# Performance work log

Measured on AMD Instinct MI355X. Metric: run time of the kernel, lower is better.

## Reference

```python
import jax, jax.numpy as jnp
import numpy as np

B, H_RES, W_RES, C, WS, SHIFT, NH = 32, 64, 64, 256, 8, 4, 8
N = WS * WS              # tokens per window
HD = C // NH             # head dim
HID = 4 * C              # mlp hidden
CPB_HID = 512            # relative-position MLP hidden


def _rel_index():
    coords = np.stack(np.meshgrid(np.arange(WS), np.arange(WS), indexing='ij'))  # [2,WS,WS]
    cf = coords.reshape(2, -1)
    rel = (cf[:, :, None] - cf[:, None, :]).transpose(1, 2, 0).astype(np.int64)  # [n,n,2]
    rel[..., 0] += WS - 1
    rel[..., 1] += WS - 1
    rel[..., 0] *= 2 * WS - 1
    return rel.sum(-1)  # [n,n] indices into (2WS-1)^2 table

REL_INDEX = _rel_index()


def _attn_mask():
    img = np.zeros((H_RES, W_RES))
    slices = (slice(0, -WS), slice(-WS, -SHIFT), slice(-SHIFT, None))
    cnt = 0
    for hs in slices:
        for ws_ in slices:
            img[hs, ws_] = cnt
            cnt += 1
    mw = img.reshape(H_RES // WS, WS, W_RES // WS, WS).transpose(0, 2, 1, 3).reshape(-1, N)
    am = mw[:, None, :] - mw[:, :, None]  # [nw,n,n]
    return np.where(am != 0, -100.0, 0.0).astype(np.float32)

ATTN_MASK = _attn_mask()


def _cpb_table():
    r = np.arange(-(WS - 1), WS, dtype=np.float32)
    t = np.stack(np.meshgrid(r, r, indexing='ij'), axis=-1)[None]  # [1,2WS-1,2WS-1,2]
    t = t / (WS - 1) * 8.0
    t = np.sign(t) * np.log2(np.abs(t) + 1.0) / np.log2(8.0)
    return t.astype(np.float32)

CPB_TABLE = _cpb_table()


def setup_inputs() -> dict:
    key = jax.random.key(0)
    ks = jax.random.split(key, 10)
    s = 0.02
    return {
        'x': jax.random.normal(ks[0], (B, H_RES * W_RES, C), jnp.float32),
        'qkv_w': jax.random.normal(ks[1], (3 * C, C), jnp.float32) * s,
        'q_bias': jnp.zeros((C,), jnp.float32),
        'v_bias': jnp.zeros((C,), jnp.float32),
        'logit_scale': jnp.full((NH, 1, 1), jnp.log(10.0), jnp.float32),
        'cpb_w1': jax.random.normal(ks[2], (CPB_HID, 2), jnp.float32) * s,
        'cpb_b1': jnp.zeros((CPB_HID,), jnp.float32),
        'cpb_w2': jax.random.normal(ks[3], (NH, CPB_HID), jnp.float32) * s,
        'proj_w': jax.random.normal(ks[4], (C, C), jnp.float32) * s,
        'proj_b': jnp.zeros((C,), jnp.float32),
        'norm1_g': jnp.ones((C,), jnp.float32),
        'norm1_b': jnp.zeros((C,), jnp.float32),
        'norm2_g': jnp.ones((C,), jnp.float32),
        'norm2_b': jnp.zeros((C,), jnp.float32),
        'fc1_w': jax.random.normal(ks[5], (HID, C), jnp.float32) * s,
        'fc1_b': jnp.zeros((HID,), jnp.float32),
        'fc2_w': jax.random.normal(ks[6], (C, HID), jnp.float32) * s,
        'fc2_b': jnp.zeros((C,), jnp.float32),
    }


def _layernorm(x, g, b, eps=1e-5):
    m = jnp.mean(x, axis=-1, keepdims=True)
    v = jnp.mean(jnp.square(x - m), axis=-1, keepdims=True)
    return (x - m) * jax.lax.rsqrt(v + eps) * g + b


def _l2norm(x, eps=1e-12):
    n = jnp.sqrt(jnp.sum(jnp.square(x), axis=-1, keepdims=True))
    return x / jnp.maximum(n, eps)


def reference(x, qkv_w, q_bias, v_bias, logit_scale, cpb_w1, cpb_b1, cpb_w2,
              proj_w, proj_b, norm1_g, norm1_b, norm2_g, norm2_b,
              fc1_w, fc1_b, fc2_w, fc2_b):
    shortcut = x
    xv = x.reshape(B, H_RES, W_RES, C)
    # cyclic shift
    sx = jnp.roll(xv, (-SHIFT, -SHIFT), axis=(1, 2))
    # window partition -> [B*nw, N, C]
    win = sx.reshape(B, H_RES // WS, WS, W_RES // WS, WS, C)
    win = win.transpose(0, 1, 3, 2, 4, 5).reshape(-1, N, C)

    # qkv with zero k-bias
    qkv_bias = jnp.concatenate([q_bias, jnp.zeros_like(v_bias), v_bias])
    qkv = win @ qkv_w.T + qkv_bias
    qkv = qkv.reshape(-1, N, 3, NH, HD).transpose(2, 0, 3, 1, 4)  # [3,Bw,NH,N,HD]
    q, k, v = qkv[0], qkv[1], qkv[2]

    # cosine attention with clamped learnable temperature
    attn = jnp.einsum('whnd,whmd->whnm', _l2norm(q), _l2norm(k))
    scale = jnp.exp(jnp.minimum(logit_scale, jnp.log(100.0)))  # [NH,1,1]
    attn = attn * scale

    # continuous relative position bias via MLP
    table = jnp.asarray(CPB_TABLE)  # [1,2WS-1,2WS-1,2]
    hmid = jax.nn.relu(table @ cpb_w1.T + cpb_b1)
    bias_table = (hmid @ cpb_w2.T).reshape(-1, NH)  # [(2WS-1)^2, NH]
    rpb = bias_table[jnp.asarray(REL_INDEX).reshape(-1)].reshape(N, N, NH)
    rpb = jax.nn.sigmoid(rpb.transpose(2, 0, 1)) * 16.0  # [NH,N,N]
    attn = attn + rpb[None]

    # shift mask
    mask = jnp.asarray(ATTN_MASK)  # [nw,N,N]
    nw = mask.shape[0]
    attn = attn.reshape(-1, nw, NH, N, N) + mask[None, :, None]
    attn = attn.reshape(-1, NH, N, N)
    attn = jax.nn.softmax(attn, axis=-1)

    out = jnp.einsum('whnm,whmd->whnd', attn, v).transpose(0, 2, 1, 3).reshape(-1, N, C)
    out = out @ proj_w.T + proj_b

    # window reverse + reverse shift
    out = out.reshape(B, H_RES // WS, W_RES // WS, WS, WS, C)
    out = out.transpose(0, 1, 3, 2, 4, 5).reshape(B, H_RES, W_RES, C)
    out = jnp.roll(out, (SHIFT, SHIFT), axis=(1, 2)).reshape(B, H_RES * W_RES, C)

    # post-norm residual (Swin v2 style)
    x1 = shortcut + _layernorm(out, norm1_g, norm1_b)
    mlp_out = jax.nn.gelu(x1 @ fc1_w.T + fc1_b, approximate=False) @ fc2_w.T + fc2_b
    x2 = x1 + _layernorm(mlp_out, norm2_g, norm2_b)
    return x2
```

## Files before the change

kernel.cpp:

```cpp
#include <hip/hip_runtime.h>

typedef unsigned short u16;
typedef unsigned int u32;
typedef __attribute__((ext_vector_type(8))) short bf16x8;
typedef __attribute__((ext_vector_type(4))) float f32x4;

#define CC_    256
#define NHD_   8
#define NT_    64
#define HD_    32
#define HID_   1024
#define CPBH_  512
#define BW_    2048
#define TOK_   131072
#define SHIFT_ 4

__device__ __forceinline__ int region9(int ph, int pw) {
  return (ph < 56 ? 0 : (ph < 60 ? 3 : 6)) + (pw < 56 ? 0 : (pw < 60 ? 1 : 2));
}
__device__ __forceinline__ float dot32(const float* qr, const float* krow) {
  float d0 = 0.f, d1 = 0.f, d2 = 0.f, d3 = 0.f;
#pragma unroll
  for (int d = 0; d < HD_; d += 4) {
    float4 kk = *reinterpret_cast<const float4*>(krow + d);
    d0 += qr[d] * kk.x; d1 += qr[d + 1] * kk.y;
    d2 += qr[d + 2] * kk.z; d3 += qr[d + 3] * kk.w;
  }
  return (d0 + d1) + (d2 + d3);
}

__device__ __forceinline__ u16 f2bf(float f) {
  u32 u = __builtin_bit_cast(u32, f);
  u = (u + 0x7FFFu + ((u >> 16) & 1u)) >> 16;
  return (u16)u;
}

__device__ __forceinline__ void split4(float4 f, uint2& hi, uint2& lo) {
  u16 h0 = f2bf(f.x), h1 = f2bf(f.y), h2 = f2bf(f.z), h3 = f2bf(f.w);
  float r0 = f.x - __builtin_bit_cast(float, (u32)h0 << 16);
  float r1 = f.y - __builtin_bit_cast(float, (u32)h1 << 16);
  float r2 = f.z - __builtin_bit_cast(float, (u32)h2 << 16);
  float r3 = f.w - __builtin_bit_cast(float, (u32)h3 << 16);
  hi = make_uint2((u32)h0 | ((u32)h1 << 16), (u32)h2 | ((u32)h3 << 16));
  lo = make_uint2((u32)f2bf(r0) | ((u32)f2bf(r1) << 16),
                  (u32)f2bf(r2) | ((u32)f2bf(r3) << 16));
}

__global__ void cpb_kernel(const float* __restrict__ w1, const float* __restrict__ b1,
                           const float* __restrict__ w2, float* __restrict__ bias_table) {
  __shared__ float hid[CPBH_];
  int p = blockIdx.x;
  int k = threadIdx.x;
  int hi = p / 15, wi = p % 15;
  float a0 = (float)(hi - 7) / 7.0f * 8.0f;
  float a1 = (float)(wi - 7) / 7.0f * 8.0f;
  float t0 = (a0 == 0.0f) ? 0.0f : copysignf(log2f(fabsf(a0) + 1.0f) / 3.0f, a0);
  float t1 = (a1 == 0.0f) ? 0.0f : copysignf(log2f(fabsf(a1) + 1.0f) / 3.0f, a1);
  float h = t0 * w1[2 * k] + t1 * w1[2 * k + 1] + b1[k];
  hid[k] = fmaxf(h, 0.0f);
  __syncthreads();
  if (k < NHD_) {
    float s = 0.0f;
    for (int j = 0; j < CPBH_; j++) s += hid[j] * w2[k * CPBH_ + j];
    bias_table[p * NHD_ + k] = s;
  }
}

__global__ void rpb_kernel(const float* __restrict__ bias_table, float* __restrict__ rpb) {
  int h = blockIdx.x >> 6;
  int i = blockIdx.x & 63;
  int j = threadIdx.x;
  int dih = (i >> 3) - (j >> 3) + 7;
  int diw = (i & 7) - (j & 7) + 7;
  float v = bias_table[(dih * 15 + diw) * NHD_ + h];
  rpb[(((h << 6) + i) << 6) + j] = 16.0f / (1.0f + expf(-v));
}

__global__ void convw_kernel(const float* __restrict__ w, u16* __restrict__ o, int n) {
  int i = blockIdx.x * 256 + threadIdx.x;
  if (i < n) o[i] = f2bf(w[i]);
}

__global__ void convsplit_kernel(const float* __restrict__ w, u16* __restrict__ hi,
                                 u16* __restrict__ lo, int n) {
  int i = blockIdx.x * 256 + threadIdx.x;
  if (i < n) {
    float v = w[i];
    u16 h = f2bf(v);
    hi[i] = h;
    lo[i] = f2bf(v - __builtin_bit_cast(float, (u32)h << 16));
  }
}

__global__ __launch_bounds__(512) void qkv_mfma_kernel(
    const float* __restrict__ x,
    const u16* __restrict__ wh_, const u16* __restrict__ wl_,
    const float* __restrict__ qb, const float* __restrict__ vb,
    float* __restrict__ qo, float* __restrict__ ko, float* __restrict__ vo, int w0) {
  __shared__ u16 xh[64 * 256];
  __shared__ u16 xl[64 * 256];
  int tid = threadIdx.x;
  int lane = tid & 63, wid = tid >> 6;
  int lr = lane & 15, lk = lane >> 4;
  int wl2 = blockIdx.x;
  int w = w0 + wl2;
  int b = w >> 6, win = w & 63, wwh = win >> 3, www = win & 7;

#pragma unroll
  for (int i = 0; i < 8; i++) {
    int idx = tid + i * 512;
    int n = idx >> 6, c4 = idx & 63;
    int sh = wwh * 8 + (n >> 3), sw = www * 8 + (n & 7);
    int hh = (sh + SHIFT_) & 63, wc = (sw + SHIFT_) & 63;
    float4 f = *reinterpret_cast<const float4*>(
        x + ((size_t)((b << 12) + (hh << 6) + wc)) * CC_ + c4 * 4);
    uint2 hi, lo; split4(f, hi, lo);
    int u = c4 >> 1;
    int off16 = n * 256 + ((u ^ (n & 7)) << 3) + ((c4 & 1) << 2);
    *reinterpret_cast<uint2*>(&xh[off16]) = hi;
    *reinterpret_cast<uint2*>(&xl[off16]) = lo;
  }
  __syncthreads();

  f32x4 acc[4][6];
#pragma unroll
  for (int m = 0; m < 4; m++)
#pragma unroll
    for (int nf = 0; nf < 6; nf++) acc[m][nf] = (f32x4){0.f, 0.f, 0.f, 0.f};

  for (int k0 = 0; k0 < CC_; k0 += 32) {
    int u0 = (k0 >> 3) + lk;
    bf16x8 ah[4], al[4];
#pragma unroll
    for (int m = 0; m < 4; m++) {
      int row = m * 16 + lr;
      int off16 = row * 256 + ((u0 ^ (row & 7)) << 3);
      ah[m] = *reinterpret_cast<const bf16x8*>(&xh[off16]);
      al[m] = *reinterpret_cast<const bf16x8*>(&xl[off16]);
    }
#pragma unroll
    for (int nf = 0; nf < 6; nf++) {
      int col = wid * 96 + nf * 16 + lr;
      size_t wo = (size_t)col * CC_ + k0 + lk * 8;
      bf16x8 bh = *reinterpret_cast<const bf16x8*>(wh_ + wo);
      bf16x8 bl = *reinterpret_cast<const bf16x8*>(wl_ + wo);
#pragma unroll
      for (int m = 0; m < 4; m++) {
        acc[m][nf] = __builtin_amdgcn_mfma_f32_16x16x32_bf16(ah[m], bh, acc[m][nf], 0, 0, 0);
        acc[m][nf] = __builtin_amdgcn_mfma_f32_16x16x32_bf16(al[m], bh, acc[m][nf], 0, 0, 0);
        acc[m][nf] = __builtin_amdgcn_mfma_f32_16x16x32_bf16(ah[m], bl, acc[m][nf], 0, 0, 0);
      }
    }
  }

#pragma unroll
  for (int nf = 0; nf < 6; nf++) {
    int col = wid * 96 + nf * 16 + lr;
    int mat = col >> 8, cc = col & 255;
    float bias = (mat == 0) ? qb[cc] : ((mat == 2) ? vb[cc] : 0.f);
    float* dst = (mat == 0) ? qo : ((mat == 1) ? ko : vo);
    int hd = cc >> 5, d = cc & 31;
    float* dp = dst + ((size_t)(wl2 * NHD_ + hd) * NT_) * HD_ + d;
#pragma unroll
    for (int m = 0; m < 4; m++)
#pragma unroll
      for (int r = 0; r < 4; r++) {
        int n = m * 16 + lk * 4 + r;
        dp[(size_t)n * HD_] = acc[m][nf][r] + bias;
      }
  }
}

__global__ __launch_bounds__(64) void attn_kernel(
    const float* __restrict__ qq, const float* __restrict__ kk_, const float* __restrict__ vv_,
    const float* __restrict__ ls, const float* __restrict__ rpb, float* __restrict__ attn_out, int w0) {
  __shared__ float ks[NT_][HD_];
  __shared__ float vs[NT_][HD_];
  int bid = blockIdx.x;
  int wl = bid >> 3, h = bid & 7;
  int w = w0 + wl;
  int i = threadIdx.x;
  size_t base = (size_t)bid * (NT_ * HD_) + (size_t)i * HD_;

  float qr[HD_];
  float ss = 0.f;
#pragma unroll
  for (int d = 0; d < HD_; d += 4) {
    float4 f = *reinterpret_cast<const float4*>(qq + base + d);
    qr[d] = f.x; qr[d + 1] = f.y; qr[d + 2] = f.z; qr[d + 3] = f.w;
    ss += f.x * f.x + f.y * f.y + f.z * f.z + f.w * f.w;
  }
  float inv = 1.0f / fmaxf(sqrtf(ss), 1e-12f);
#pragma unroll
  for (int d = 0; d < HD_; d++) qr[d] *= inv;

  float kr[HD_]; ss = 0.f;
#pragma unroll
  for (int d = 0; d < HD_; d += 4) {
    float4 f = *reinterpret_cast<const float4*>(kk_ + base + d);
    kr[d] = f.x; kr[d + 1] = f.y; kr[d + 2] = f.z; kr[d + 3] = f.w;
    ss += f.x * f.x + f.y * f.y + f.z * f.z + f.w * f.w;
  }
  inv = 1.0f / fmaxf(sqrtf(ss), 1e-12f);
#pragma unroll
  for (int d = 0; d < HD_; d += 4) {
    float4 t; t.x = kr[d] * inv; t.y = kr[d + 1] * inv; t.z = kr[d + 2] * inv; t.w = kr[d + 3] * inv;
    *reinterpret_cast<float4*>(&ks[i][d]) = t;
  }
#pragma unroll
  for (int d = 0; d < HD_; d += 4) {
    float4 f = *reinterpret_cast<const float4*>(vv_ + base + d);
    *reinterpret_cast<float4*>(&vs[i][d]) = f;
  }
  __syncthreads();

  float scale = expf(fminf(ls[h], 4.605170185988091f));
  const float* rp = rpb + (((h << 6) + i) << 6);
  int win = w & 63, wh = win >> 3, ww = win & 7;
  int regi = region9(wh * 8 + (i >> 3), ww * 8 + (i & 7));

  float m = -1e30f, l = 0.f;
  for (int j = 0; j < NT_; j++) {
    float dot = dot32(qr, &ks[j][0]);
    int regj = region9(wh * 8 + (j >> 3), ww * 8 + (j & 7));
    float val = dot * scale + rp[j] + (regj == regi ? 0.f : -100.f);
    float nm = fmaxf(m, val);
    l = l * expf(m - nm) + expf(val - nm);
    m = nm;
  }
  float rl = 1.0f / l;

  float acc[HD_];
#pragma unroll
  for (int d = 0; d < HD_; d++) acc[d] = 0.f;
  for (int j = 0; j < NT_; j++) {
    float dot = dot32(qr, &ks[j][0]);
    int regj = region9(wh * 8 + (j >> 3), ww * 8 + (j & 7));
    float val = dot * scale + rp[j] + (regj == regi ? 0.f : -100.f);
    float p = expf(val - m) * rl;
#pragma unroll
    for (int d = 0; d < HD_; d += 4) {
      float4 vvv = *reinterpret_cast<const float4*>(&vs[j][d]);
      acc[d] += p * vvv.x; acc[d + 1] += p * vvv.y; acc[d + 2] += p * vvv.z; acc[d + 3] += p * vvv.w;
    }
  }
  float* op = attn_out + ((size_t)(wl * NT_ + i)) * CC_ + h * HD_;
#pragma unroll
  for (int d = 0; d < HD_; d += 4) {
    float4 t; t.x = acc[d]; t.y = acc[d + 1]; t.z = acc[d + 2]; t.w = acc[d + 3];
    *reinterpret_cast<float4*>(op + d) = t;
  }
}

__global__ __launch_bounds__(512) void proj_mfma_kernel(
    const float* __restrict__ attn_out,
    const u16* __restrict__ pwh, const u16* __restrict__ pwl, const float* __restrict__ pb,
    const float* __restrict__ g, const float* __restrict__ bb,
    const float* __restrict__ x, float* __restrict__ x1, int w0) {
  __shared__ union {
    struct { u16 ah[64 * 256]; u16 al[64 * 256]; } s;
    float po[64][CC_];
  } sm;
  int tid = threadIdx.x;
  int lane = tid & 63, wid = tid >> 6;
  int lr = lane & 15, lk = lane >> 4;
  int wl2 = blockIdx.x;
  int w = w0 + wl2;

#pragma unroll
  for (int i = 0; i < 8; i++) {
    int idx = tid + i * 512;
    int n = idx >> 6, c4 = idx & 63;
    float4 f = *reinterpret_cast<const float4*>(
        attn_out + ((size_t)(wl2 * NT_ + n)) * CC_ + c4 * 4);
    uint2 hi, lo; split4(f, hi, lo);
    int u = c4 >> 1;
    int off16 = n * 256 + ((u ^ (n & 7)) << 3) + ((c4 & 1) << 2);
    *reinterpret_cast<uint2*>(&sm.s.ah[off16]) = hi;
    *reinterpret_cast<uint2*>(&sm.s.al[off16]) = lo;
  }
  __syncthreads();

  f32x4 acc[4][2];
#pragma unroll
  for (int m = 0; m < 4; m++)
#pragma unroll
    for (int nf = 0; nf < 2; nf++) acc[m][nf] = (f32x4){0.f, 0.f, 0.f, 0.f};

  for (int k0 = 0; k0 < CC_; k0 += 32) {
    int u0 = (k0 >> 3) + lk;
    bf16x8 ah[4], al[4];
#pragma unroll
    for (int m = 0; m < 4; m++) {
      int row = m * 16 + lr;
      int off16 = row * 256 + ((u0 ^ (row & 7)) << 3);
      ah[m] = *reinterpret_cast<const bf16x8*>(&sm.s.ah[off16]);
      al[m] = *reinterpret_cast<const bf16x8*>(&sm.s.al[off16]);
    }
#pragma unroll
    for (int nf = 0; nf < 2; nf++) {
      int col = wid * 32 + nf * 16 + lr;
      size_t wo = (size_t)col * CC_ + k0 + lk * 8;
      bf16x8 bh = *reinterpret_cast<const bf16x8*>(pwh + wo);
      bf16x8 bl = *reinterpret_cast<const bf16x8*>(pwl + wo);
#pragma unroll
      for (int m = 0; m < 4; m++) {
        acc[m][nf] = __builtin_amdgcn_mfma_f32_16x16x32_bf16(ah[m], bh, acc[m][nf], 0, 0, 0);
        acc[m][nf] = __builtin_amdgcn_mfma_f32_16x16x32_bf16(al[m], bh, acc[m][nf], 0, 0, 0);
        acc[m][nf] = __builtin_amdgcn_mfma_f32_16x16x32_bf16(ah[m], bl, acc[m][nf], 0, 0, 0);
      }
    }
  }
  __syncthreads();

#pragma unroll
  for (int nf = 0; nf < 2; nf++) {
    int col = wid * 32 + nf * 16 + lr;
    float bv = pb[col];
#pragma unroll
    for (int m = 0; m < 4; m++)
#pragma unroll
      for (int r = 0; r < 4; r++)
        sm.po[m * 16 + lk * 4 + r][col] = acc[m][nf][r] + bv;
  }
  __syncthreads();

  int t = wid * 8 + (lane >> 3);
  int j8 = ((lane & 7) + (lane >> 3)) & 7;
  float4 pv[8];
  float sum = 0.f, sq = 0.f;
#pragma unroll
  for (int i = 0; i < 8; i++) {
    float4 v = *reinterpret_cast<const float4*>(&sm.po[t][j8 * 4 + i * 32]);
    pv[i] = v;
    sum += v.x + v.y + v.z + v.w;
    sq += v.x * v.x + v.y * v.y + v.z * v.z + v.w * v.w;
  }
#pragma unroll
  for (int off = 1; off < 8; off <<= 1) {
    sum += __shfl_xor(sum, off, 8);
    sq  += __shfl_xor(sq, off, 8);
  }
  float mean = sum * (1.0f / CC_);
  float var = sq * (1.0f / CC_) - mean * mean;
  float rs = rsqrtf(fmaxf(var, 0.0f) + 1e-5f);
  int b = w >> 6, win = w & 63, wwh = win >> 3, www = win & 7;
  int sh = wwh * 8 + (t >> 3), sw = www * 8 + (t & 7);
  int hh = (sh + SHIFT_) & 63, wc = (sw + SHIFT_) & 63;
  size_t tok = ((size_t)(b << 12)) + (hh << 6) + wc;
  const float* xrow = x + tok * CC_;
  float* orow = x1 + tok * CC_;
#pragma unroll
  for (int i = 0; i < 8; i++) {
    int c = j8 * 4 + i * 32;
    float4 xg = *reinterpret_cast<const float4*>(xrow + c);
    float4 gg = *reinterpret_cast<const float4*>(g + c);
    float4 bv = *reinterpret_cast<const float4*>(bb + c);
    float4 r;
    r.x = xg.x + (pv[i].x - mean) * rs * gg.x + bv.x;
    r.y = xg.y + (pv[i].y - mean) * rs * gg.y + bv.y;
    r.z = xg.z + (pv[i].z - mean) * rs * gg.z + bv.z;
    r.w = xg.w + (pv[i].w - mean) * rs * gg.w + bv.w;
    *reinterpret_cast<float4*>(orow + c) = r;
  }
}

#define BM_   64

__global__ __launch_bounds__(512) void mlp_mfma_kernel(
    const float* __restrict__ x1,
    const u16* __restrict__ w1bf, const float* __restrict__ b1,
    const u16* __restrict__ w2bf, const float* __restrict__ b2,
    const float* __restrict__ g, const float* __restrict__ bb,
    float* __restrict__ out) {
  __shared__ union {
    struct { u16 xs[64 * 256]; u16 hid[2][64 * 128]; } s;
    float po[BM_][CC_];
  } sm;

  int tid = threadIdx.x;
  int lane = tid & 63;
  int wid = tid >> 6;
  int lr = lane & 15;
  int lk = lane >> 4;
  int whid = wid >> 1;
  int wtok = wid & 1;
  int wout = wid >> 1;
  int wtk2 = wid & 1;
  size_t t0 = (size_t)blockIdx.x * BM_;

#pragma unroll
  for (int i = 0; i < 8; i++) {
    int idx = tid + i * 512;
    int row = idx >> 6;
    int c4 = idx & 63;
    float4 f = *reinterpret_cast<const float4*>(x1 + (t0 + row) * CC_ + c4 * 4);
    u32 p0 = (u32)f2bf(f.x) | ((u32)f2bf(f.y) << 16);
    u32 p1 = (u32)f2bf(f.z) | ((u32)f2bf(f.w) << 16);
    int u = c4 >> 1;
    int off16 = row * 256 + ((u ^ (row & 7)) << 3) + ((c4 & 1) << 2);
    *reinterpret_cast<uint2*>(&sm.s.xs[off16]) = make_uint2(p0, p1);
  }

  f32x4 acc2[2][4];
#pragma unroll
  for (int mf = 0; mf < 2; mf++)
#pragma unroll
    for (int nf = 0; nf < 4; nf++) acc2[mf][nf] = (f32x4){0.f, 0.f, 0.f, 0.f};

  auto FC1 = [&](int ch) {
    int h0 = ch * 128;
    f32x4 acc1[2][2];
#pragma unroll
    for (int hf = 0; hf < 2; hf++)
#pragma unroll
      for (int tf = 0; tf < 2; tf++) acc1[hf][tf] = (f32x4){0.f, 0.f, 0.f, 0.f};
#pragma unroll
    for (int k0 = 0; k0 < CC_; k0 += 32) {
      bf16x8 a0 = *reinterpret_cast<const bf16x8*>(
          w1bf + (size_t)(h0 + whid * 32 + lr) * CC_ + k0 + lk * 8);
      bf16x8 a1 = *reinterpret_cast<const bf16x8*>(
          w1bf + (size_t)(h0 + whid * 32 + 16 + lr) * CC_ + k0 + lk * 8);
      int u0 = (k0 >> 3) + lk;
      int r0 = wtok * 32 + lr;
      int r1 = wtok * 32 + 16 + lr;
      bf16x8 bx0 = *reinterpret_cast<const bf16x8*>(&sm.s.xs[r0 * 256 + ((u0 ^ (r0 & 7)) << 3)]);
      bf16x8 bx1 = *reinterpret_cast<const bf16x8*>(&sm.s.xs[r1 * 256 + ((u0 ^ (r1 & 7)) << 3)]);
      acc1[0][0] = __builtin_amdgcn_mfma_f32_16x16x32_bf16(a0, bx0, acc1[0][0], 0, 0, 0);
      acc1[0][1] = __builtin_amdgcn_mfma_f32_16x16x32_bf16(a0, bx1, acc1[0][1], 0, 0, 0);
      acc1[1][0] = __builtin_amdgcn_mfma_f32_16x16x32_bf16(a1, bx0, acc1[1][0], 0, 0, 0);
      acc1[1][1] = __builtin_amdgcn_mfma_f32_16x16x32_bf16(a1, bx1, acc1[1][1], 0, 0, 0);
    }
    u16* hb = &sm.s.hid[ch & 1][0];
#pragma unroll
    for (int hf = 0; hf < 2; hf++) {
      float4 bq = *reinterpret_cast<const float4*>(b1 + h0 + whid * 32 + hf * 16 + lk * 4);
      int col = whid * 32 + hf * 16 + lk * 4;
      int u = col >> 3;
      int half4 = (lk & 1) << 2;
#pragma unroll
      for (int tf = 0; tf < 2; tf++) {
        int token = wtok * 32 + tf * 16 + lr;
        float v0 = acc1[hf][tf][0] + bq.x;
        float v1 = acc1[hf][tf][1] + bq.y;
        float v2 = acc1[hf][tf][2] + bq.z;
        float v3 = acc1[hf][tf][3] + bq.w;
        v0 = 0.5f * v0 * (1.0f + erff(v0 * 0.7071067811865475f));
        v1 = 0.5f * v1 * (1.0f + erff(v1 * 0.7071067811865475f));
        v2 = 0.5f * v2 * (1.0f + erff(v2 * 0.7071067811865475f));
        v3 = 0.5f * v3 * (1.0f + erff(v3 * 0.7071067811865475f));
        u32 p0 = (u32)f2bf(v0) | ((u32)f2bf(v1) << 16);
        u32 p1 = (u32)f2bf(v2) | ((u32)f2bf(v3) << 16);
        int off16 = token * 128 + ((u ^ (token & 7)) << 3) + half4;
        *reinterpret_cast<uint2*>(&hb[off16]) = make_uint2(p0, p1);
      }
    }
  };

  auto FC2 = [&](int ch) {
    int h0 = ch * 128;
    const u16* hb = &sm.s.hid[ch & 1][0];
#pragma unroll
    for (int kk = 0; kk < 128; kk += 32) {
      int u0 = (kk >> 3) + lk;
      int r0 = wtk2 * 32 + lr;
      int r1 = wtk2 * 32 + 16 + lr;
      bf16x8 a0 = *reinterpret_cast<const bf16x8*>(&hb[r0 * 128 + ((u0 ^ (r0 & 7)) << 3)]);
      bf16x8 a1 = *reinterpret_cast<const bf16x8*>(&hb[r1 * 128 + ((u0 ^ (r1 & 7)) << 3)]);
#pragma unroll
      for (int nf = 0; nf < 4; nf++) {
        bf16x8 bf = *reinterpret_cast<const bf16x8*>(
            w2bf + (size_t)(wout * 64 + nf * 16 + lr) * HID_ + h0 + kk + lk * 8);
        acc2[0][nf] = __builtin_amdgcn_mfma_f32_16x16x32_bf16(a0, bf, acc2[0][nf], 0, 0, 0);
        acc2[1][nf] = __builtin_amdgcn_mfma_f32_16x16x32_bf16(a1, bf, acc2[1][nf], 0, 0, 0);
      }
    }
  };

  __syncthreads();
  FC1(0);
  __syncthreads();
  for (int ch = 0; ch < 8; ch++) {
    if (ch < 7) FC1(ch + 1);
    FC2(ch);
    __syncthreads();
  }

#pragma unroll
  for (int mf = 0; mf < 2; mf++)
#pragma unroll
    for (int nf = 0; nf < 4; nf++) {
      int col = wout * 64 + nf * 16 + lr;
      float bv = b2[col];
#pragma unroll
      for (int r = 0; r < 4; r++) {
        int row = wtk2 * 32 + mf * 16 + lk * 4 + r;
        sm.po[row][col] = acc2[mf][nf][r] + bv;
      }
    }
  __syncthreads();

  int t = wid * 8 + (lane >> 3);
  int j8 = ((lane & 7) + (lane >> 3)) & 7;
  float4 pv[8];
  float sum = 0.f, sq = 0.f;
#pragma unroll
  for (int i = 0; i < 8; i++) {
    float4 v = *reinterpret_cast<const float4*>(&sm.po[t][j8 * 4 + i * 32]);
    pv[i] = v;
    sum += v.x + v.y + v.z + v.w;
    sq += v.x * v.x + v.y * v.y + v.z * v.z + v.w * v.w;
  }
#pragma unroll
  for (int off = 1; off < 8; off <<= 1) {
    sum += __shfl_xor(sum, off, 8);
    sq  += __shfl_xor(sq, off, 8);
  }
  float mean = sum * (1.0f / CC_);
  float var = sq * (1.0f / CC_) - mean * mean;
  float rs = rsqrtf(fmaxf(var, 0.0f) + 1e-5f);
  const float* xrow = x1 + (t0 + t) * CC_;
  float* orow = out + (t0 + t) * CC_;
#pragma unroll
  for (int i = 0; i < 8; i++) {
    int c = j8 * 4 + i * 32;
    float4 xg = *reinterpret_cast<const float4*>(xrow + c);
    float4 gg = *reinterpret_cast<const float4*>(g + c);
    float4 bv = *reinterpret_cast<const float4*>(bb + c);
    float4 r;
    r.x = xg.x + (pv[i].x - mean) * rs * gg.x + bv.x;
    r.y = xg.y + (pv[i].y - mean) * rs * gg.y + bv.y;
    r.z = xg.z + (pv[i].z - mean) * rs * gg.z + bv.z;
    r.w = xg.w + (pv[i].w - mean) * rs * gg.w + bv.w;
    *reinterpret_cast<float4*>(orow + c) = r;
  }
}

extern "C" void kernel_launch(void* const* d_in, const int* in_sizes, int n_in,
                              void* d_out, int out_size, void* d_ws, size_t ws_size,
                              hipStream_t stream) {
  const float* x       = (const float*)d_in[0];
  const float* qkv_w   = (const float*)d_in[1];
  const float* q_bias  = (const float*)d_in[2];
  const float* v_bias  = (const float*)d_in[3];
  const float* logit_s = (const float*)d_in[4];
  const float* cpb_w1  = (const float*)d_in[5];
  const float* cpb_b1  = (const float*)d_in[6];
  const float* cpb_w2  = (const float*)d_in[7];
  const float* proj_w  = (const float*)d_in[8];
  const float* proj_b  = (const float*)d_in[9];
  const float* n1g     = (const float*)d_in[10];
  const float* n1b     = (const float*)d_in[11];
  const float* n2g     = (const float*)d_in[12];
  const float* n2b     = (const float*)d_in[13];
  const float* fc1_w   = (const float*)d_in[14];
  const float* fc1_b   = (const float*)d_in[15];
  const float* fc2_w   = (const float*)d_in[16];
  const float* fc2_b   = (const float*)d_in[17];
  float* out = (float*)d_out;
  char* ws = (char*)d_ws;

  u16* fc1bf = (u16*)(ws + 139264);
  u16* fc2bf = (u16*)(ws + 663552);
  u16* qwh   = (u16*)(ws + 1187840);
  u16* qwl   = (u16*)(ws + 1581056);
  u16* pwh   = (u16*)(ws + 1974272);
  u16* pwl   = (u16*)(ws + 2105344);
  const size_t OFF_CH = 2236416;
  const size_t ELEM_PER_WIN = (size_t)NHD_ * NT_ * HD_;
  const size_t PER_WIN_BYTES = 4 * ELEM_PER_WIN * 4;

  float* bias_table = (float*)(ws);
  float* rpb        = (float*)(ws + 8192);

  long long avail = (long long)ws_size - (long long)OFF_CH;
  long long ncw = avail / (long long)PER_WIN_BYTES;
  if (ncw < 1) ncw = 1;
  if (ncw > BW_) ncw = BW_;
  int nc = (int)ncw;

  float* qc = (float*)(ws + OFF_CH);
  float* kc = qc + (size_t)nc * ELEM_PER_WIN;
  float* vc = kc + (size_t)nc * ELEM_PER_WIN;
  float* ac = vc + (size_t)nc * ELEM_PER_WIN;

  cpb_kernel<<<225, 512, 0, stream>>>(cpb_w1, cpb_b1, cpb_w2, bias_table);
  rpb_kernel<<<NHD_ * NT_, 64, 0, stream>>>(bias_table, rpb);
  convw_kernel<<<1024, 256, 0, stream>>>(fc1_w, fc1bf, HID_ * CC_);
  convw_kernel<<<1024, 256, 0, stream>>>(fc2_w, fc2bf, CC_ * HID_);
  convsplit_kernel<<<768, 256, 0, stream>>>(qkv_w, qwh, qwl, 3 * CC_ * CC_);
  convsplit_kernel<<<256, 256, 0, stream>>>(proj_w, pwh, pwl, CC_ * CC_);

  for (int w0 = 0; w0 < BW_; w0 += nc) {
    int nw = (BW_ - w0 < nc) ? (BW_ - w0) : nc;
    qkv_mfma_kernel<<<nw, 512, 0, stream>>>(x, qwh, qwl, q_bias, v_bias, qc, kc, vc, w0);
    attn_kernel<<<nw * 8, 64, 0, stream>>>(qc, kc, vc, logit_s, rpb, ac, w0);
    proj_mfma_kernel<<<nw, 512, 0, stream>>>(ac, pwh, pwl, proj_b, n1g, n1b, x, out, w0);
  }
  mlp_mfma_kernel<<<TOK_ / BM_, 512, 0, stream>>>(out, fc1bf, fc1_b, fc2bf, fc2_b, n2g, n2b, out);
}
```

Baseline: 1.673 ms.

## Use single-pass softmax with bounded max, transpose rpb, cache FC1 activations in registers

The attention kernel drops the first online-softmax pass. It subtracts a fixed upper bound (scale+16) instead of the running max, so each score is computed once and normalised at the end. The rpb table is stored transposed so that adjacent threads (rows i) read contiguous addresses for each j, giving coalesced loads. In the MLP kernel, the LDS-resident x1 fragments for FC1 are loaded once into registers and reused across all eight hidden chunks instead of being re-read from LDS every chunk. Risks are exp underflow when real scores sit far below the bound (masked entries are -100 anyway) and higher register pressure in the MLP kernel.

```diff
diff --git a/kernel.cpp b/kernel.cpp
--- a/kernel.cpp
+++ b/kernel.cpp
@@ -68,12 +68,12 @@
 
 __global__ void rpb_kernel(const float* __restrict__ bias_table, float* __restrict__ rpb) {
   int h = blockIdx.x >> 6;
-  int i = blockIdx.x & 63;
-  int j = threadIdx.x;
+  int j = blockIdx.x & 63;
+  int i = threadIdx.x;
   int dih = (i >> 3) - (j >> 3) + 7;
   int diw = (i & 7) - (j & 7) + 7;
   float v = bias_table[(dih * 15 + diw) * NHD_ + h];
-  rpb[(((h << 6) + i) << 6) + j] = 16.0f / (1.0f + expf(-v));
+  rpb[(((h << 6) + j) << 6) + i] = 16.0f / (1.0f + expf(-v));
 }
 
 __global__ void convw_kernel(const float* __restrict__ w, u16* __restrict__ o, int n) {
@@ -173,7 +173,7 @@
 
 __global__ __launch_bounds__(64) void attn_kernel(
     const float* __restrict__ qq, const float* __restrict__ kk_, const float* __restrict__ vv_,
-    const float* __restrict__ ls, const float* __restrict__ rpb, float* __restrict__ attn_out, int w0) {
+    const float* __restrict__ ls, const float* __restrict__ rpbT, float* __restrict__ attn_out, int w0) {
   __shared__ float ks[NT_][HD_];
   __shared__ float vs[NT_][HD_];
   int bid = blockIdx.x;
@@ -215,39 +215,33 @@
   __syncthreads();
 
   float scale = expf(fminf(ls[h], 4.605170185988091f));
-  const float* rp = rpb + (((h << 6) + i) << 6);
+  float M = scale + 16.0f;
+  const float* rpT = rpbT + ((h << 6) << 6) + i;
   int win = w & 63, wh = win >> 3, ww = win & 7;
   int regi = region9(wh * 8 + (i >> 3), ww * 8 + (i & 7));
 
-  float m = -1e30f, l = 0.f;
-  for (int j = 0; j < NT_; j++) {
-    float dot = dot32(qr, &ks[j][0]);
-    int regj = region9(wh * 8 + (j >> 3), ww * 8 + (j & 7));
-    float val = dot * scale + rp[j] + (regj == regi ? 0.f : -100.f);
-    float nm = fmaxf(m, val);
-    l = l * expf(m - nm) + expf(val - nm);
-    m = nm;
-  }
-  float rl = 1.0f / l;
-
+  float l = 0.f;
   float acc[HD_];
 #pragma unroll
   for (int d = 0; d < HD_; d++) acc[d] = 0.f;
   for (int j = 0; j < NT_; j++) {
     float dot = dot32(qr, &ks[j][0]);
     int regj = region9(wh * 8 + (j >> 3), ww * 8 + (j & 7));
-    float val = dot * scale + rp[j] + (regj == regi ? 0.f : -100.f);
-    float p = expf(val - m) * rl;
+    float val = dot * scale + rpT[j << 6] + (regj == regi ? 0.f : -100.f);
+    float p = expf(val - M);
+    l += p;
 #pragma unroll
     for (int d = 0; d < HD_; d += 4) {
       float4 vvv = *reinterpret_cast<const float4*>(&vs[j][d]);
       acc[d] += p * vvv.x; acc[d + 1] += p * vvv.y; acc[d + 2] += p * vvv.z; acc[d + 3] += p * vvv.w;
     }
   }
+  float rl = 1.0f / l;
+
   float* op = attn_out + ((size_t)(wl * NT_ + i)) * CC_ + h * HD_;
 #pragma unroll
   for (int d = 0; d < HD_; d += 4) {
-    float4 t; t.x = acc[d]; t.y = acc[d + 1]; t.z = acc[d + 2]; t.w = acc[d + 3];
+    float4 t; t.x = acc[d] * rl; t.y = acc[d + 1] * rl; t.z = acc[d + 2] * rl; t.w = acc[d + 3] * rl;
     *reinterpret_cast<float4*>(op + d) = t;
   }
 }
@@ -408,6 +402,19 @@
 #pragma unroll
     for (int nf = 0; nf < 4; nf++) acc2[mf][nf] = (f32x4){0.f, 0.f, 0.f, 0.f};
 
+  __syncthreads();
+
+  bf16x8 bx[8][2];
+#pragma unroll
+  for (int k0i = 0; k0i < 8; k0i++) {
+    int u0 = k0i * 4 + lk;
+#pragma unroll
+    for (int tf = 0; tf < 2; tf++) {
+      int rr = wtok * 32 + tf * 16 + lr;
+      bx[k0i][tf] = *reinterpret_cast<const bf16x8*>(&sm.s.xs[rr * 256 + ((u0 ^ (rr & 7)) << 3)]);
+    }
+  }
+
   auto FC1 = [&](int ch) {
     int h0 = ch * 128;
     f32x4 acc1[2][2];
@@ -416,20 +423,16 @@
 #pragma unroll
       for (int tf = 0; tf < 2; tf++) acc1[hf][tf] = (f32x4){0.f, 0.f, 0.f, 0.f};
 #pragma unroll
-    for (int k0 = 0; k0 < CC_; k0 += 32) {
+    for (int k0i = 0; k0i < 8; k0i++) {
+      int k0 = k0i * 32;
       bf16x8 a0 = *reinterpret_cast<const bf16x8*>(
           w1bf + (size_t)(h0 + whid * 32 + lr) * CC_ + k0 + lk * 8);
       bf16x8 a1 = *reinterpret_cast<const bf16x8*>(
           w1bf + (size_t)(h0 + whid * 32 + 16 + lr) * CC_ + k0 + lk * 8);
-      int u0 = (k0 >> 3) + lk;
-      int r0 = wtok * 32 + lr;
-      int r1 = wtok * 32 + 16 + lr;
-      bf16x8 bx0 = *reinterpret_cast<const bf16x8*>(&sm.s.xs[r0 * 256 + ((u0 ^ (r0 & 7)) << 3)]);
-      bf16x8 bx1 = *reinterpret_cast<const bf16x8*>(&sm.s.xs[r1 * 256 + ((u0 ^ (r1 & 7)) << 3)]);
-      acc1[0][0] = __builtin_amdgcn_mfma_f32_16x16x32_bf16(a0, bx0, acc1[0][0], 0, 0, 0);
-      acc1[0][1] = __builtin_amdgcn_mfma_f32_16x16x32_bf16(a0, bx1, acc1[0][1], 0, 0, 0);
-      acc1[1][0] = __builtin_amdgcn_mfma_f32_16x16x32_bf16(a1, bx0, acc1[1][0], 0, 0, 0);
-      acc1[1][1] = __builtin_amdgcn_mfma_f32_16x16x32_bf16(a1, bx1, acc1[1][1], 0, 0, 0);
+      acc1[0][0] = __builtin_amdgcn_mfma_f32_16x16x32_bf16(a0, bx[k0i][0], acc1[0][0], 0, 0, 0);
+      acc1[0][1] = __builtin_amdgcn_mfma_f32_16x16x32_bf16(a0, bx[k0i][1], acc1[0][1], 0, 0, 0);
+      acc1[1][0] = __builtin_amdgcn_mfma_f32_16x16x32_bf16(a1, bx[k0i][0], acc1[1][0], 0, 0, 0);
+      acc1[1][1] = __builtin_amdgcn_mfma_f32_16x16x32_bf16(a1, bx[k0i][1], acc1[1][1], 0, 0, 0);
     }
     u16* hb = &sm.s.hid[ch & 1][0];
 #pragma unroll
@@ -477,7 +480,6 @@
     }
   };
 
-  __syncthreads();
   FC1(0);
   __syncthreads();
   for (int ch = 0; ch < 8; ch++) {
```

After: 1.646 ms. Within noise of the previous version (-1.7%).
